# Performance work log

Hardware: AMD Instinct MI355X
Metric: run time of the kernel (lower is better)

Reference implementation:

```python
import jax, jax.numpy as jnp
import numpy as np

N_NODES = 50000
N_EDGES = 600000
D_IN = 128
D_OUT = 128


def setup_inputs() -> dict:
    key = jax.random.key(0)
    k1, k2, k3, k4 = jax.random.split(key, 4)
    x = jax.random.normal(k1, (N_NODES, D_IN), dtype=jnp.float32)
    edge_index = jax.random.randint(k2, (2, N_EDGES), 0, N_NODES, dtype=jnp.int64)
    edge_weight = jax.random.uniform(k3, (N_EDGES,), dtype=jnp.float32)
    W = jax.random.normal(k4, (D_IN, D_OUT), dtype=jnp.float32) * (1.0 / np.sqrt(D_IN))
    b = jnp.zeros((D_OUT,), dtype=jnp.float32)
    return {"x": x, "edge_index": edge_index, "edge_weight": edge_weight, "W": W, "b": b}


def reference(x, edge_index, edge_weight, W, b):
    # GCNConv (PyG semantics): add self-loops, symmetric deg^{-1/2} normalization,
    # linear transform, scatter-add to targets, bias; then ReLU. Dropout is
    # identity in eval mode.
    n = x.shape[0]
    loop = jnp.arange(n, dtype=edge_index.dtype)
    src = jnp.concatenate([edge_index[0], loop])  # message sources
    dst = jnp.concatenate([edge_index[1], loop])  # aggregation targets
    ew = jnp.concatenate([edge_weight, jnp.ones((n,), dtype=x.dtype)])
    # weighted in-degree on targets
    deg = jax.ops.segment_sum(ew, dst, num_segments=n)
    dinv = jnp.where(deg > 0, jax.lax.rsqrt(deg), jnp.zeros_like(deg))
    norm = dinv[src] * ew * dinv[dst]  # [E+N]
    h = x @ W  # [N, D_OUT]
    msg = h[src] * norm[:, None]  # [E+N, D_OUT]
    out = jax.ops.segment_sum(msg, dst, num_segments=n) + b
    return jax.nn.relu(out)
```

## Files before the change

### kernel.cpp

```cpp
#include <hip/hip_runtime.h>

#define N_NODES 50000
#define N_EDGES 600000
#define D 128
#define SCAN_B 256
#define NB ((N_NODES + SCAN_B - 1) / SCAN_B)
#define REP 4
#define FXSHIFT 44

typedef __attribute__((ext_vector_type(8))) short short8;
typedef __attribute__((ext_vector_type(4))) float f32x4;
typedef unsigned long long u64;

__device__ __forceinline__ ushort f2bf(float f) {
    unsigned u = __float_as_uint(f);
    unsigned r = (u + 0x7FFFu + ((u >> 16) & 1u)) >> 16;
    return (ushort)r;
}
__device__ __forceinline__ float bf2f(ushort h) {
    return __uint_as_float(((unsigned)h) << 16);
}

__global__ void zero_kernel(ulonglong2* __restrict__ p, int n2) {
    int i = blockIdx.x * 256 + threadIdx.x;
    if (i < n2) p[i] = make_ulonglong2(0ull, 0ull);
}

__global__ void deg_cnt_kernel(const int* __restrict__ dst,
                               const float* __restrict__ ew,
                               u64* __restrict__ degp) {
    int e = blockIdx.x * 256 + threadIdx.x;
    if (e < N_EDGES) {
        int d = dst[e];
        int r = blockIdx.x & (REP - 1);
        u64 fx = (u64)llrintf(ew[e] * 16777216.0f);
        atomicAdd(&degp[(size_t)r * N_NODES + d], (1ull << FXSHIFT) | fx);
    }
}

__global__ void scan1_kernel(const u64* __restrict__ degp,
                             float* __restrict__ dinv,
                             int* __restrict__ cnt,
                             int* __restrict__ blockSums) {
    __shared__ int s[SCAN_B];
    int t = threadIdx.x;
    int i = blockIdx.x * SCAN_B + t;
    int v = 0;
    if (i < N_NODES) {
        u64 fxsum = 0;
        int c = 0;
#pragma unroll
        for (int r = 0; r < REP; ++r) {
            u64 p = degp[(size_t)r * N_NODES + i];
            fxsum += p & ((1ull << FXSHIFT) - 1);
            c += (int)(p >> FXSHIFT);
        }
        float deg = 1.0f + (float)fxsum * (1.0f / 16777216.0f);
        dinv[i] = rsqrtf(deg);
        v = c;
    }
    s[t] = v;
    __syncthreads();
    for (int o = 1; o < SCAN_B; o <<= 1) {
        int x = (t >= o) ? s[t - o] : 0;
        __syncthreads();
        s[t] += x;
        __syncthreads();
    }
    if (i < N_NODES) cnt[i] = s[t] - v;
    if (t == SCAN_B - 1) blockSums[blockIdx.x] = s[t];
}

__global__ void scan3_kernel(const u64* __restrict__ degp,
                             const int* __restrict__ cnt,
                             const int* __restrict__ blockSums,
                             int* __restrict__ off,
                             int* __restrict__ cursor) {
    __shared__ int sbase;
    if (threadIdx.x == 0) {
        int s = 0;
        for (int r = 0; r < blockIdx.x; ++r) s += blockSums[r];
        sbase = s;
    }
    __syncthreads();
    int i = blockIdx.x * SCAN_B + threadIdx.x;
    if (i < N_NODES) {
        int o = cnt[i] + sbase;
        off[i] = o;
        int run = o;
#pragma unroll
        for (int r = 0; r < REP; ++r) {
            cursor[(size_t)r * N_NODES + i] = run;
            run += (int)(degp[(size_t)r * N_NODES + i] >> FXSHIFT);
        }
    }
    if (i == 0) off[N_NODES] = N_EDGES;
}

__global__ void fill_kernel(const int* __restrict__ src, const int* __restrict__ dst,
                            const float* __restrict__ ew, const float* __restrict__ dinv,
                            int* __restrict__ cursor,
                            u64* __restrict__ edge_s) {
    int e = blockIdx.x * 256 + threadIdx.x;
    if (e >= N_EDGES) return;
    int s = src[e];
    int d = dst[e];
    int r = blockIdx.x & (REP - 1);
    int pos = atomicAdd(&cursor[(size_t)r * N_NODES + d], 1);
    float w = ew[e] * dinv[s] * dinv[d];
    edge_s[pos] = ((u64)__float_as_uint(w) << 32) | (unsigned)s;
}

__global__ void wfrag_kernel(const float* __restrict__ W,
                             ushort* __restrict__ wfh, ushort* __restrict__ wfl) {
    int t = blockIdx.x * 256 + threadIdx.x;
    int lane = t & 63;
    int ks   = (t >> 6) & 3;
    int ct   = t >> 8;
    int n  = ct * 16 + (lane & 15);
    int k0 = ks * 32 + (lane >> 4) * 8;
    ushort hv[8], lv[8];
#pragma unroll
    for (int j = 0; j < 8; ++j) {
        float v = W[(k0 + j) * D + n];
        ushort hh = f2bf(v);
        hv[j] = hh;
        lv[j] = f2bf(v - bf2f(hh));
    }
    size_t base = (((size_t)ct * 4 + ks) * 64 + lane) * 8;
#pragma unroll
    for (int j = 0; j < 8; ++j) { wfh[base + j] = hv[j]; wfl[base + j] = lv[j]; }
}

__global__ __launch_bounds__(256) void gemm_mfma_kernel(
        const float* __restrict__ x,
        const ushort* __restrict__ wfh, const ushort* __restrict__ wfl,
        ushort* __restrict__ hbf) {
    __shared__ __attribute__((aligned(16))) ushort xh[64 * 128];

    int t  = threadIdx.x;
    int r0 = blockIdx.x * 64;

#pragma unroll
    for (int p = 0; p < 8; ++p) {
        int row  = p * 8 + (t >> 5);
        int g    = t & 31;
        int grow = r0 + row;
        float4 v = make_float4(0.f, 0.f, 0.f, 0.f);
        if (grow < N_NODES) v = ((const float4*)(x + (size_t)grow * D))[g];
        ushort4 hi;
        hi.x = f2bf(v.x); hi.y = f2bf(v.y); hi.z = f2bf(v.z); hi.w = f2bf(v.w);
        int bo = (row * 256 + g * 8) ^ ((row & 7) << 4);
        *(ushort4*)((char*)xh + bo) = hi;
    }
    __syncthreads();

    int w  = t >> 6;
    int l  = t & 63;
    int m  = l & 15;
    int gq = l >> 4;

    f32x4 acc[8];
#pragma unroll
    for (int ct = 0; ct < 8; ++ct) acc[ct] = (f32x4){0.f, 0.f, 0.f, 0.f};

#pragma unroll
    for (int ks = 0; ks < 4; ++ks) {
        int row = w * 16 + m;
        int bo  = (row * 256 + gq * 16 + ks * 64) ^ ((row & 7) << 4);
        short8 ah = *(const short8*)((const char*)xh + bo);
#pragma unroll
        for (int ct = 0; ct < 8; ++ct) {
            size_t fb = (((size_t)ct * 4 + ks) * 64 + l) * 8;
            short8 bh = *(const short8*)(wfh + fb);
            short8 bl = *(const short8*)(wfl + fb);
            acc[ct] = __builtin_amdgcn_mfma_f32_16x16x32_bf16(ah, bh, acc[ct], 0, 0, 0);
            acc[ct] = __builtin_amdgcn_mfma_f32_16x16x32_bf16(ah, bl, acc[ct], 0, 0, 0);
        }
    }

    int orow0 = r0 + w * 16 + gq * 4;
#pragma unroll
    for (int ct = 0; ct < 8; ++ct) {
#pragma unroll
        for (int r = 0; r < 4; ++r) {
            int row = orow0 + r;
            if (row < N_NODES) hbf[(size_t)row * D + ct * 16 + m] = f2bf(acc[ct][r]);
        }
    }
}

__global__ __launch_bounds__(256) void gather_kernel(
        const int* __restrict__ off, const u64* __restrict__ edge_s,
        const float* __restrict__ dinv,
        const ushort* __restrict__ hbf, const float* __restrict__ b,
        float* __restrict__ out) {
    int node = blockIdx.x * 4 + (threadIdx.x >> 6);
    if (node >= N_NODES) return;
    int lane = threadIdx.x & 63;
    int q  = lane >> 4;
    int fl = lane & 15;

    int begin = off[node];
    int end   = off[node + 1];
    float dd  = dinv[node];
    float sw  = dd * dd;

    float acc[8] = {0.f, 0.f, 0.f, 0.f, 0.f, 0.f, 0.f, 0.f};

    short8 sv = ((const short8*)(hbf + (size_t)node * D))[fl];
    if (q == 0) {
#pragma unroll
        for (int j = 0; j < 8; ++j) acc[j] = bf2f((ushort)sv[j]) * sw;
    }

    for (int j0 = begin; j0 < end; j0 += 64) {
        int nc = end - j0;
        if (nc > 64) nc = 64;
        u64 p = 0;
        if (lane < nc) p = edge_s[j0 + lane];
        int iters = (nc + 3) >> 2;
#pragma unroll 2
        for (int t = 0; t < iters; ++t) {
            int ei = t * 4 + q;
            u64 pe = __shfl((long long)p, ei);
            bool valid = ei < nc;
            int   ss = valid ? (int)(pe & 0xFFFFFFFFu) : 0;
            float ww = valid ? __uint_as_float((unsigned)(pe >> 32)) : 0.0f;
            short8 v = ((const short8*)(hbf + (size_t)ss * D))[fl];
#pragma unroll
            for (int j = 0; j < 8; ++j)
                acc[j] = fmaf(bf2f((ushort)v[j]), ww, acc[j]);
        }
    }

#pragma unroll
    for (int j = 0; j < 8; ++j) {
        acc[j] += __shfl_xor(acc[j], 16);
        acc[j] += __shfl_xor(acc[j], 32);
    }

    if (q == 0) {
        float4 b1 = ((const float4*)b)[fl * 2];
        float4 b2 = ((const float4*)b)[fl * 2 + 1];
        float4 o1 = make_float4(fmaxf(acc[0] + b1.x, 0.f), fmaxf(acc[1] + b1.y, 0.f),
                                fmaxf(acc[2] + b1.z, 0.f), fmaxf(acc[3] + b1.w, 0.f));
        float4 o2 = make_float4(fmaxf(acc[4] + b2.x, 0.f), fmaxf(acc[5] + b2.y, 0.f),
                                fmaxf(acc[6] + b2.z, 0.f), fmaxf(acc[7] + b2.w, 0.f));
        ((float4*)(out + (size_t)node * D))[fl * 2]     = o1;
        ((float4*)(out + (size_t)node * D))[fl * 2 + 1] = o2;
    }
}

__global__ void fb_init_kernel(float* __restrict__ deg) {
    int i = blockIdx.x * 256 + threadIdx.x;
    if (i < N_NODES) deg[i] = 1.0f;
}
__global__ void fb_deg_kernel(const int* __restrict__ dst, const float* __restrict__ ew,
                              float* __restrict__ deg) {
    int e = blockIdx.x * 256 + threadIdx.x;
    if (e < N_EDGES) atomicAdd(&deg[dst[e]], ew[e]);
}
__global__ void fb_dinv_kernel(const float* __restrict__ deg, float* __restrict__ dinv) {
    int i = blockIdx.x * 256 + threadIdx.x;
    if (i < N_NODES) {
        float d = deg[i];
        dinv[i] = (d > 0.0f) ? rsqrtf(d) : 0.0f;
    }
}
__global__ void fb_gemm_kernel(const float* __restrict__ x, const float* __restrict__ W,
                               float* __restrict__ h) {
    __shared__ float xs[2][D];
    int lr  = threadIdx.x >> 7;
    int col = threadIdx.x & 127;
    int row = blockIdx.x * 2 + lr;
    if (row < N_NODES) xs[lr][col] = x[(size_t)row * D + col];
    __syncthreads();
    if (row >= N_NODES) return;
    float acc = 0.0f;
#pragma unroll 8
    for (int k = 0; k < D; ++k) acc = fmaf(xs[lr][k], W[k * D + col], acc);
    h[(size_t)row * D + col] = acc;
}
__global__ void fb_scatter_kernel(const int* __restrict__ src, const int* __restrict__ dst,
                                  const float* __restrict__ ew, const float* __restrict__ dinv,
                                  const float* __restrict__ h, float* __restrict__ acc) {
    int e = blockIdx.x * 4 + (threadIdx.x >> 6);
    if (e >= N_EDGES) return;
    int lane = threadIdx.x & 63;
    int s = src[e];
    int d = dst[e];
    float w = ew[e] * dinv[s] * dinv[d];
    float2 v = ((const float2*)(h + (size_t)s * D))[lane];
    float* ap = acc + (size_t)d * D + lane * 2;
    atomicAdd(ap,     v.x * w);
    atomicAdd(ap + 1, v.y * w);
}
__global__ void fb_finalize_kernel(const float* __restrict__ h, const float* __restrict__ dinv,
                                   const float* __restrict__ b, float* __restrict__ out) {
    int i = blockIdx.x * 256 + threadIdx.x;
    if (i >= N_NODES * D) return;
    int node = i >> 7;
    int col  = i & 127;
    float di = dinv[node];
    float v = out[i] + h[i] * di * di + b[col];
    out[i] = fmaxf(v, 0.0f);
}

extern "C" void kernel_launch(void* const* d_in, const int* in_sizes, int n_in,
                              void* d_out, int out_size, void* d_ws, size_t ws_size,
                              hipStream_t stream) {
    const float* x  = (const float*)d_in[0];
    const int*   ei = (const int*)d_in[1];
    const float* ew = (const float*)d_in[2];
    const float* W  = (const float*)d_in[3];
    const float* b  = (const float*)d_in[4];
    float*       out = (float*)d_out;

    const int* src = ei;
    const int* dst = ei + N_EDGES;

    ushort* hbf      = (ushort*)d_ws;
    u64*    degp     = (u64*)(hbf + (size_t)N_NODES * D);
    float*  dinv     = (float*)(degp + (size_t)REP * N_NODES);
    int*    cnt      = (int*)(dinv + N_NODES);
    int*    off      = cnt + N_NODES;
    int*    blockSums= off + (N_NODES + 1);
    int*    cursor   = blockSums + SCAN_B;
    u64*    edge_s   = (u64*)(cursor + (size_t)REP * N_NODES);
    ushort* wfh      = (ushort*)(edge_s + N_EDGES);
    ushort* wfl      = wfh + 16384;
    size_t need = ((size_t)(wfl + 16384) - (size_t)d_ws);

    if (ws_size >= need) {
        int n2 = (REP * N_NODES) / 2;
        zero_kernel<<<(n2 + 255) / 256, 256, 0, stream>>>((ulonglong2*)degp, n2);

        deg_cnt_kernel<<<(N_EDGES + 255) / 256, 256, 0, stream>>>(dst, ew, degp);
        scan1_kernel<<<NB, SCAN_B, 0, stream>>>(degp, dinv, cnt, blockSums);
        scan3_kernel<<<NB, SCAN_B, 0, stream>>>(degp, cnt, blockSums, off, cursor);

        fill_kernel<<<(N_EDGES + 255) / 256, 256, 0, stream>>>(src, dst, ew, dinv,
                                                               cursor, edge_s);

        wfrag_kernel<<<8, 256, 0, stream>>>(W, wfh, wfl);
        gemm_mfma_kernel<<<(N_NODES + 63) / 64, 256, 0, stream>>>(x, wfh, wfl, hbf);

        gather_kernel<<<(N_NODES + 3) / 4, 256, 0, stream>>>(off, edge_s, dinv,
                                                             hbf, b, out);
    } else {
        float* h    = (float*)d_ws;
        float* deg  = h + (size_t)N_NODES * D;
        float* dv   = deg + N_NODES;
        hipMemsetAsync(d_out, 0, (size_t)out_size * sizeof(float), stream);
        fb_init_kernel<<<(N_NODES + 255) / 256, 256, 0, stream>>>(deg);
        fb_deg_kernel<<<(N_EDGES + 255) / 256, 256, 0, stream>>>(dst, ew, deg);
        fb_dinv_kernel<<<(N_NODES + 255) / 256, 256, 0, stream>>>(deg, dv);
        fb_gemm_kernel<<<(N_NODES + 1) / 2, 256, 0, stream>>>(x, W, h);
        fb_scatter_kernel<<<(N_EDGES + 3) / 4, 256, 0, stream>>>(src, dst, ew, dv, h, out);
        fb_finalize_kernel<<<(N_NODES * D + 255) / 256, 256, 0, stream>>>(h, dv, b, out);
    }
}
```

Baseline: 123.7 us.

## Merge prep, scan, and fill/GEMM launches to cut kernel count

Folds the W-fragment conversion into the zeroing kernel and merges the two scan kernels into one decoupled-lookback scan that uses global flag words. The CSR fill and the MFMA GEMM now run as one launch with a block-index split, so the GEMM can overlap the atomic scatter. This removes several kernel launches and serialization gaps. The lookback relies on earlier blocks being scheduled first, which is not guaranteed, and the flags region is zeroed together with degp.

```diff
diff --git a/kernel.cpp b/kernel.cpp
--- a/kernel.cpp
+++ b/kernel.cpp
@@ -7,6 +7,9 @@
 #define NB ((N_NODES + SCAN_B - 1) / SCAN_B)
 #define REP 4
 #define FXSHIFT 44
+#define GEMM_BLOCKS ((N_NODES + 63) / 64)
+#define FILL_BLOCKS ((N_EDGES + 255) / 256)
+#define ZERO_BLOCKS 392
 
 typedef __attribute__((ext_vector_type(8))) short short8;
 typedef __attribute__((ext_vector_type(4))) float f32x4;
@@ -21,9 +24,36 @@
     return __uint_as_float(((unsigned)h) << 16);
 }
 
-__global__ void zero_kernel(ulonglong2* __restrict__ p, int n2) {
-    int i = blockIdx.x * 256 + threadIdx.x;
-    if (i < n2) p[i] = make_ulonglong2(0ull, 0ull);
+__device__ __forceinline__ void wfrag_body(int t, const float* __restrict__ W,
+                                           ushort* __restrict__ wfh,
+                                           ushort* __restrict__ wfl) {
+    int lane = t & 63;
+    int ks   = (t >> 6) & 3;
+    int ct   = t >> 8;
+    int n  = ct * 16 + (lane & 15);
+    int k0 = ks * 32 + (lane >> 4) * 8;
+    ushort hv[8], lv[8];
+#pragma unroll
+    for (int j = 0; j < 8; ++j) {
+        float v = W[(k0 + j) * D + n];
+        ushort hh = f2bf(v);
+        hv[j] = hh;
+        lv[j] = f2bf(v - bf2f(hh));
+    }
+    size_t base = (((size_t)ct * 4 + ks) * 64 + lane) * 8;
+#pragma unroll
+    for (int j = 0; j < 8; ++j) { wfh[base + j] = hv[j]; wfl[base + j] = lv[j]; }
+}
+
+__global__ void prep_kernel(ulonglong2* __restrict__ zp, int n2,
+                            const float* __restrict__ W,
+                            ushort* __restrict__ wfh, ushort* __restrict__ wfl) {
+    if (blockIdx.x < ZERO_BLOCKS) {
+        int i = blockIdx.x * 256 + threadIdx.x;
+        if (i < n2) zp[i] = make_ulonglong2(0ull, 0ull);
+    } else {
+        wfrag_body((blockIdx.x - ZERO_BLOCKS) * 256 + threadIdx.x, W, wfh, wfl);
+    }
 }
 
 __global__ void deg_cnt_kernel(const int* __restrict__ dst,
@@ -38,22 +68,25 @@
     }
 }
 
-__global__ void scan1_kernel(const u64* __restrict__ degp,
-                             float* __restrict__ dinv,
-                             int* __restrict__ cnt,
-                             int* __restrict__ blockSums) {
+__global__ void scan_fused_kernel(const u64* __restrict__ degp,
+                                  float* __restrict__ dinv,
+                                  int* __restrict__ off,
+                                  int* __restrict__ cursor,
+                                  u64* __restrict__ flags) {
     __shared__ int s[SCAN_B];
+    __shared__ int sbase_sh;
     int t = threadIdx.x;
     int i = blockIdx.x * SCAN_B + t;
     int v = 0;
+    u64 pr[REP];
     if (i < N_NODES) {
         u64 fxsum = 0;
         int c = 0;
 #pragma unroll
         for (int r = 0; r < REP; ++r) {
-            u64 p = degp[(size_t)r * N_NODES + i];
-            fxsum += p & ((1ull << FXSHIFT) - 1);
-            c += (int)(p >> FXSHIFT);
+            pr[r] = degp[(size_t)r * N_NODES + i];
+            fxsum += pr[r] & ((1ull << FXSHIFT) - 1);
+            c += (int)(pr[r] >> FXSHIFT);
         }
         float deg = 1.0f + (float)fxsum * (1.0f / 16777216.0f);
         dinv[i] = rsqrtf(deg);
@@ -67,126 +100,112 @@
         s[t] += x;
         __syncthreads();
     }
-    if (i < N_NODES) cnt[i] = s[t] - v;
-    if (t == SCAN_B - 1) blockSums[blockIdx.x] = s[t];
-}
-
-__global__ void scan3_kernel(const u64* __restrict__ degp,
-                             const int* __restrict__ cnt,
-                             const int* __restrict__ blockSums,
-                             int* __restrict__ off,
-                             int* __restrict__ cursor) {
-    __shared__ int sbase;
-    if (threadIdx.x == 0) {
-        int s = 0;
-        for (int r = 0; r < blockIdx.x; ++r) s += blockSums[r];
-        sbase = s;
+    int localExcl = s[t] - v;
+    int blockSum  = s[SCAN_B - 1];
+
+    if (t == 0) {
+        u64 agg = (u64)blockSum;
+        int sb = 0;
+        if (blockIdx.x == 0) {
+            atomicExch(&flags[0], (2ull << 62) | agg);
+        } else {
+            atomicExch(&flags[blockIdx.x], (1ull << 62) | agg);
+            u64 run = 0;
+            for (int j = blockIdx.x - 1; j >= 0; --j) {
+                u64 f;
+                do { f = atomicAdd(&flags[j], 0ull); } while ((f >> 62) == 0ull);
+                run += f & ((1ull << 62) - 1);
+                if ((f >> 62) == 2ull) break;
+            }
+            sb = (int)run;
+            atomicExch(&flags[blockIdx.x], (2ull << 62) | (agg + (u64)sb));
+        }
+        sbase_sh = sb;
     }
     __syncthreads();
-    int i = blockIdx.x * SCAN_B + threadIdx.x;
+
     if (i < N_NODES) {
-        int o = cnt[i] + sbase;
+        int o = localExcl + sbase_sh;
         off[i] = o;
         int run = o;
 #pragma unroll
         for (int r = 0; r < REP; ++r) {
             cursor[(size_t)r * N_NODES + i] = run;
-            run += (int)(degp[(size_t)r * N_NODES + i] >> FXSHIFT);
+            run += (int)(pr[r] >> FXSHIFT);
         }
     }
     if (i == 0) off[N_NODES] = N_EDGES;
 }
 
-__global__ void fill_kernel(const int* __restrict__ src, const int* __restrict__ dst,
-                            const float* __restrict__ ew, const float* __restrict__ dinv,
-                            int* __restrict__ cursor,
-                            u64* __restrict__ edge_s) {
-    int e = blockIdx.x * 256 + threadIdx.x;
-    if (e >= N_EDGES) return;
-    int s = src[e];
-    int d = dst[e];
-    int r = blockIdx.x & (REP - 1);
-    int pos = atomicAdd(&cursor[(size_t)r * N_NODES + d], 1);
-    float w = ew[e] * dinv[s] * dinv[d];
-    edge_s[pos] = ((u64)__float_as_uint(w) << 32) | (unsigned)s;
-}
-
-__global__ void wfrag_kernel(const float* __restrict__ W,
-                             ushort* __restrict__ wfh, ushort* __restrict__ wfl) {
-    int t = blockIdx.x * 256 + threadIdx.x;
-    int lane = t & 63;
-    int ks   = (t >> 6) & 3;
-    int ct   = t >> 8;
-    int n  = ct * 16 + (lane & 15);
-    int k0 = ks * 32 + (lane >> 4) * 8;
-    ushort hv[8], lv[8];
-#pragma unroll
-    for (int j = 0; j < 8; ++j) {
-        float v = W[(k0 + j) * D + n];
-        ushort hh = f2bf(v);
-        hv[j] = hh;
-        lv[j] = f2bf(v - bf2f(hh));
-    }
-    size_t base = (((size_t)ct * 4 + ks) * 64 + lane) * 8;
-#pragma unroll
-    for (int j = 0; j < 8; ++j) { wfh[base + j] = hv[j]; wfl[base + j] = lv[j]; }
-}
-
-__global__ __launch_bounds__(256) void gemm_mfma_kernel(
+__global__ __launch_bounds__(256) void fused_fg_kernel(
         const float* __restrict__ x,
         const ushort* __restrict__ wfh, const ushort* __restrict__ wfl,
-        ushort* __restrict__ hbf) {
+        ushort* __restrict__ hbf,
+        const int* __restrict__ src, const int* __restrict__ dst,
+        const float* __restrict__ ew, const float* __restrict__ dinv,
+        int* __restrict__ cursor, u64* __restrict__ edge_s) {
     __shared__ __attribute__((aligned(16))) ushort xh[64 * 128];
 
-    int t  = threadIdx.x;
-    int r0 = blockIdx.x * 64;
-
-#pragma unroll
-    for (int p = 0; p < 8; ++p) {
-        int row  = p * 8 + (t >> 5);
-        int g    = t & 31;
-        int grow = r0 + row;
-        float4 v = make_float4(0.f, 0.f, 0.f, 0.f);
-        if (grow < N_NODES) v = ((const float4*)(x + (size_t)grow * D))[g];
-        ushort4 hi;
-        hi.x = f2bf(v.x); hi.y = f2bf(v.y); hi.z = f2bf(v.z); hi.w = f2bf(v.w);
-        int bo = (row * 256 + g * 8) ^ ((row & 7) << 4);
-        *(ushort4*)((char*)xh + bo) = hi;
-    }
-    __syncthreads();
-
-    int w  = t >> 6;
-    int l  = t & 63;
-    int m  = l & 15;
-    int gq = l >> 4;
-
-    f32x4 acc[8];
-#pragma unroll
-    for (int ct = 0; ct < 8; ++ct) acc[ct] = (f32x4){0.f, 0.f, 0.f, 0.f};
-
-#pragma unroll
-    for (int ks = 0; ks < 4; ++ks) {
-        int row = w * 16 + m;
-        int bo  = (row * 256 + gq * 16 + ks * 64) ^ ((row & 7) << 4);
-        short8 ah = *(const short8*)((const char*)xh + bo);
+    int t = threadIdx.x;
+    if (blockIdx.x < GEMM_BLOCKS) {
+        int r0 = blockIdx.x * 64;
+#pragma unroll
+        for (int p = 0; p < 8; ++p) {
+            int row  = p * 8 + (t >> 5);
+            int g    = t & 31;
+            int grow = r0 + row;
+            float4 v = make_float4(0.f, 0.f, 0.f, 0.f);
+            if (grow < N_NODES) v = ((const float4*)(x + (size_t)grow * D))[g];
+            ushort4 hi;
+            hi.x = f2bf(v.x); hi.y = f2bf(v.y); hi.z = f2bf(v.z); hi.w = f2bf(v.w);
+            int bo = (row * 256 + g * 8) ^ ((row & 7) << 4);
+            *(ushort4*)((char*)xh + bo) = hi;
+        }
+        __syncthreads();
+
+        int w  = t >> 6;
+        int l  = t & 63;
+        int m  = l & 15;
+        int gq = l >> 4;
+
+        f32x4 acc[8];
+#pragma unroll
+        for (int ct = 0; ct < 8; ++ct) acc[ct] = (f32x4){0.f, 0.f, 0.f, 0.f};
+
+#pragma unroll
+        for (int ks = 0; ks < 4; ++ks) {
+            int row = w * 16 + m;
+            int bo  = (row * 256 + gq * 16 + ks * 64) ^ ((row & 7) << 4);
+            short8 ah = *(const short8*)((const char*)xh + bo);
+#pragma unroll
+            for (int ct = 0; ct < 8; ++ct) {
+                size_t fb = (((size_t)ct * 4 + ks) * 64 + l) * 8;
+                short8 bh = *(const short8*)(wfh + fb);
+                short8 bl = *(const short8*)(wfl + fb);
+                acc[ct] = __builtin_amdgcn_mfma_f32_16x16x32_bf16(ah, bh, acc[ct], 0, 0, 0);
+                acc[ct] = __builtin_amdgcn_mfma_f32_16x16x32_bf16(ah, bl, acc[ct], 0, 0, 0);
+            }
+        }
+
+        int orow0 = r0 + w * 16 + gq * 4;
 #pragma unroll
         for (int ct = 0; ct < 8; ++ct) {
-            size_t fb = (((size_t)ct * 4 + ks) * 64 + l) * 8;
-            short8 bh = *(const short8*)(wfh + fb);
-            short8 bl = *(const short8*)(wfl + fb);
-            acc[ct] = __builtin_amdgcn_mfma_f32_16x16x32_bf16(ah, bh, acc[ct], 0, 0, 0);
-            acc[ct] = __builtin_amdgcn_mfma_f32_16x16x32_bf16(ah, bl, acc[ct], 0, 0, 0);
-        }
-    }
-
-    int orow0 = r0 + w * 16 + gq * 4;
-#pragma unroll
-    for (int ct = 0; ct < 8; ++ct) {
-#pragma unroll
-        for (int r = 0; r < 4; ++r) {
-            int row = orow0 + r;
-            if (row < N_NODES) hbf[(size_t)row * D + ct * 16 + m] = f2bf(acc[ct][r]);
-        }
+#pragma unroll
+            for (int r = 0; r < 4; ++r) {
+                int row = orow0 + r;
+                if (row < N_NODES) hbf[(size_t)row * D + ct * 16 + m] = f2bf(acc[ct][r]);
+            }
+        }
+    } else {
+        int fb = blockIdx.x - GEMM_BLOCKS;
+        int e = fb * 256 + t;
+        if (e >= N_EDGES) return;
+        int s = src[e];
+        int d = dst[e];
+        int r = fb & (REP - 1);
+        int pos = atomicAdd(&cursor[(size_t)r * N_NODES + d], 1);
+        float w = ew[e] * dinv[s] * dinv[d];
+        edge_s[pos] = ((u64)__float_as_uint(w) << 32) | (unsigned)s;
     }
 }
 
@@ -320,31 +339,28 @@
     const int* src = ei;
     const int* dst = ei + N_EDGES;
 
-    ushort* hbf      = (ushort*)d_ws;
-    u64*    degp     = (u64*)(hbf + (size_t)N_NODES * D);
-    float*  dinv     = (float*)(degp + (size_t)REP * N_NODES);
-    int*    cnt      = (int*)(dinv + N_NODES);
-    int*    off      = cnt + N_NODES;
-    int*    blockSums= off + (N_NODES + 1);
-    int*    cursor   = blockSums + SCAN_B;
-    u64*    edge_s   = (u64*)(cursor + (size_t)REP * N_NODES);
-    ushort* wfh      = (ushort*)(edge_s + N_EDGES);
-    ushort* wfl      = wfh + 16384;
+    ushort* hbf    = (ushort*)d_ws;
+    u64*    degp   = (u64*)(hbf + (size_t)N_NODES * D);
+    u64*    flags  = degp + (size_t)REP * N_NODES;
+    float*  dinv   = (float*)(flags + 256);
+    int*    off    = (int*)(dinv + N_NODES);
+    int*    cursor = off + (N_NODES + 2);
+    u64*    edge_s = (u64*)(cursor + (size_t)REP * N_NODES);
+    ushort* wfh    = (ushort*)(edge_s + N_EDGES);
+    ushort* wfl    = wfh + 16384;
     size_t need = ((size_t)(wfl + 16384) - (size_t)d_ws);
 
     if (ws_size >= need) {
-        int n2 = (REP * N_NODES) / 2;
-        zero_kernel<<<(n2 + 255) / 256, 256, 0, stream>>>((ulonglong2*)degp, n2);
-
-        deg_cnt_kernel<<<(N_EDGES + 255) / 256, 256, 0, stream>>>(dst, ew, degp);
-        scan1_kernel<<<NB, SCAN_B, 0, stream>>>(degp, dinv, cnt, blockSums);
-        scan3_kernel<<<NB, SCAN_B, 0, stream>>>(degp, cnt, blockSums, off, cursor);
-
-        fill_kernel<<<(N_EDGES + 255) / 256, 256, 0, stream>>>(src, dst, ew, dinv,
-                                                               cursor, edge_s);
-
-        wfrag_kernel<<<8, 256, 0, stream>>>(W, wfh, wfl);
-        gemm_mfma_kernel<<<(N_NODES + 63) / 64, 256, 0, stream>>>(x, wfh, wfl, hbf);
+        int n2 = (int)(((size_t)REP * N_NODES * 8 + 256 * 8) / 16);
+        prep_kernel<<<ZERO_BLOCKS + 8, 256, 0, stream>>>((ulonglong2*)degp, n2,
+                                                         W, wfh, wfl);
+
+        deg_cnt_kernel<<<FILL_BLOCKS, 256, 0, stream>>>(dst, ew, degp);
+
+        scan_fused_kernel<<<NB, SCAN_B, 0, stream>>>(degp, dinv, off, cursor, flags);
+
+        fused_fg_kernel<<<GEMM_BLOCKS + FILL_BLOCKS, 256, 0, stream>>>(
+            x, wfh, wfl, hbf, src, dst, ew, dinv, cursor, edge_s);
 
         gather_kernel<<<(N_NODES + 3) / 4, 256, 0, stream>>>(off, edge_s, dinv,
                                                              hbf, b, out);
```

Result: faster. 113.2 us (-8.5%).
